# Performance work log

Hardware: AMD Instinct MI355X
Metric: run time of the kernel (lower is better)

Reference implementation:

```python
import jax, jax.numpy as jnp
import numpy as np

LN_EPS = 1e-5


def setup_inputs() -> dict:
    key = jax.random.key(0)
    ks = jax.random.split(key, 6)
    B, I, H = 16384, 512, 512
    x = jax.random.normal(ks[0], (B, I), dtype=jnp.float32)
    h_prev = jax.random.normal(ks[1], (B, H), dtype=jnp.float32)
    c_prev = jax.random.normal(ks[2], (B, H), dtype=jnp.float32)
    # packed gate weights in i|f|g|o order (equivalent to 8 separate matmuls)
    W_i = jax.random.normal(ks[3], (I, 4 * H), dtype=jnp.float32) * (1.0 / np.sqrt(I))
    W_h = jax.random.normal(ks[4], (H, 4 * H), dtype=jnp.float32) * (1.0 / np.sqrt(H))
    # biases: b_i=0, b_f=1, b_g=0, b_o=0 as in the torch module
    b = jnp.concatenate([jnp.zeros(H), jnp.ones(H), jnp.zeros(H), jnp.zeros(H)]).astype(jnp.float32)
    ln_weight = jnp.ones((H,), dtype=jnp.float32)
    ln_bias = jnp.zeros((H,), dtype=jnp.float32)
    return {"x": x, "h_prev": h_prev, "c_prev": c_prev, "W_i": W_i, "W_h": W_h,
            "b": b, "ln_weight": ln_weight, "ln_bias": ln_bias}


def layer_norm(h, w, bias):
    mu = jnp.mean(h, axis=-1, keepdims=True)
    var = jnp.var(h, axis=-1, keepdims=True)
    return (h - mu) * jax.lax.rsqrt(var + LN_EPS) * w + bias


def reference(x, h_prev, c_prev, W_i, W_h, b, ln_weight, ln_bias):
    H = h_prev.shape[-1]
    # two fused GEMMs covering all 4 gates: [B, 4H]
    gates = x @ W_i + h_prev @ W_h + b
    i, f, g, o = jnp.split(gates, 4, axis=-1)
    i = jax.nn.sigmoid(i)
    f = jax.nn.sigmoid(f)
    g = jnp.tanh(g)
    o = jax.nn.sigmoid(o)
    c = f * c_prev + i * g
    h = o * jnp.tanh(c)
    h = layer_norm(h, ln_weight, ln_bias)
    return (h, c)
```

## Files before the change

kernel.cpp:

```cpp
#include <hip/hip_runtime.h>
#include <cstdint>
#include <cstddef>

typedef unsigned short ushort_t;
typedef __attribute__((ext_vector_type(8))) short bf16x8;
typedef __attribute__((ext_vector_type(4))) float f32x4;

#define MROWS 16384
#define KDIM  1024
#define NDIM  2048
#define HDIM  512

static __device__ __forceinline__ unsigned short f2bf(float f) {
    unsigned int u = __float_as_uint(f);
    u += 0x7fffu + ((u >> 16) & 1u);
    return (unsigned short)(u >> 16);
}

static __device__ __forceinline__ float sigmoid_f(float x) {
    return 1.0f / (1.0f + __expf(-x));
}
static __device__ __forceinline__ float tanh_f(float x) {
    float t = __expf(2.0f * x);
    return 1.0f - 2.0f / (t + 1.0f);
}

__global__ __launch_bounds__(256) void pack_ab(const float* __restrict__ x,
                                               const float* __restrict__ hp,
                                               const float* __restrict__ Wi,
                                               const float* __restrict__ Wh,
                                               ushort_t* __restrict__ A,
                                               ushort_t* __restrict__ Bt) {
    __shared__ ushort_t sm[64][72];
    const int tid = threadIdx.x;
    if (blockIdx.x < 8192) {
        int t = blockIdx.x * 256 + tid;
        int row = t >> 7;
        int kc = (t & 127) << 3;
        const float* src = (kc < 512) ? (x + (size_t)row * 512 + kc)
                                      : (hp + (size_t)row * 512 + (kc - 512));
        float4 v0 = ((const float4*)src)[0];
        float4 v1 = ((const float4*)src)[1];
        ushort_t o[8] __attribute__((aligned(16)));
        o[0] = f2bf(v0.x); o[1] = f2bf(v0.y); o[2] = f2bf(v0.z); o[3] = f2bf(v0.w);
        o[4] = f2bf(v1.x); o[5] = f2bf(v1.y); o[6] = f2bf(v1.z); o[7] = f2bf(v1.w);
        *((uint4*)(A + (size_t)row * KDIM + kc)) = *((const uint4*)o);
    } else {
        int b2 = blockIdx.x - 8192;
        int kt = b2 >> 5;
        int ct = b2 & 31;
        const float* W = (kt < 8) ? (Wi + (size_t)(kt * 64) * NDIM)
                                  : (Wh + (size_t)((kt - 8) * 64) * NDIM);
        int c0 = (tid & 15) * 4;
        int r0 = tid >> 4;
#pragma unroll
        for (int r = 0; r < 4; ++r) {
            int krow = r * 16 + r0;
            float4 v = *((const float4*)(W + (size_t)krow * NDIM + ct * 64 + c0));
            sm[krow][c0 + 0] = f2bf(v.x);
            sm[krow][c0 + 1] = f2bf(v.y);
            sm[krow][c0 + 2] = f2bf(v.z);
            sm[krow][c0 + 3] = f2bf(v.w);
        }
        __syncthreads();
        int g = (ct * 64) >> 9;
        int h0 = ct * 64 - g * 512;
#pragma unroll
        for (int q = tid; q < 512; q += 256) {
            int cc = q >> 3;
            int kc = (q & 7) * 8;
            ushort_t o[8] __attribute__((aligned(16)));
#pragma unroll
            for (int j = 0; j < 8; ++j) o[j] = sm[kc + j][cc];
            int np = 4 * (h0 + cc) + g;
            *((uint4*)(Bt + (size_t)np * KDIM + kt * 64 + kc)) = *((const uint4*)o);
        }
    }
}

__global__ __launch_bounds__(256) void gemm_cell(const ushort_t* __restrict__ A,
                                                 const ushort_t* __restrict__ Bt,
                                                 const float* __restrict__ b,
                                                 const float* __restrict__ c_prev,
                                                 float* __restrict__ h_out,
                                                 float* __restrict__ c_out) {
    __shared__ float smem_f[8192];
    ushort_t* Als = (ushort_t*)smem_f;
    ushort_t* Bls = Als + 128 * 64;

    const int tid  = threadIdx.x;
    const int w    = tid >> 6;
    const int lane = tid & 63;
    const int n0 = blockIdx.x * 128;
    const int m0 = blockIdx.y * 128;
    const int wm = (w >> 1) * 64;
    const int wn = (w & 1) * 64;
    const int lr   = lane & 15;
    const int quad = lane >> 4;
    const int sw   = lr & 7;

    f32x4 zero = {0.f, 0.f, 0.f, 0.f};
    f32x4 acc[4][4];
#pragma unroll
    for (int i = 0; i < 4; ++i)
#pragma unroll
        for (int j = 0; j < 4; ++j) acc[i][j] = zero;

    for (int kt = 0; kt < KDIM / 64; ++kt) {
#pragma unroll
        for (int r = 0; r < 4; ++r) {
            int c = r * 256 + tid;
            int trow = c >> 3;
            int chg = (c & 7) ^ (trow & 7);
            const ushort_t* ga = A + (size_t)(m0 + trow) * KDIM + kt * 64 + chg * 8;
            __builtin_amdgcn_global_load_lds(
                (const __attribute__((address_space(1))) void*)ga,
                (__attribute__((address_space(3))) void*)((char*)Als + c * 16),
                16, 0, 0);
            const ushort_t* gb = Bt + (size_t)(n0 + trow) * KDIM + kt * 64 + chg * 8;
            __builtin_amdgcn_global_load_lds(
                (const __attribute__((address_space(1))) void*)gb,
                (__attribute__((address_space(3))) void*)((char*)Bls + c * 16),
                16, 0, 0);
        }
        __syncthreads();

#pragma unroll
        for (int kk = 0; kk < 2; ++kk) {
            bf16x8 af[4], bf[4];
#pragma unroll
            for (int t2 = 0; t2 < 4; ++t2) {
                int ra = wm + t2 * 16 + lr;
                int rb = wn + t2 * 16 + lr;
                int ch = kk * 4 + quad;
                af[t2] = *((const bf16x8*)(Als + (ra * 8 + (ch ^ sw)) * 8));
                bf[t2] = *((const bf16x8*)(Bls + (rb * 8 + (ch ^ sw)) * 8));
            }
#pragma unroll
            for (int tm = 0; tm < 4; ++tm)
#pragma unroll
                for (int tn = 0; tn < 4; ++tn)
                    acc[tm][tn] = __builtin_amdgcn_mfma_f32_16x16x32_bf16(
                        af[tm], bf[tn], acc[tm][tn], 0, 0, 0);
        }
        __syncthreads();
    }

#pragma unroll
    for (int half = 0; half < 2; ++half) {
        __syncthreads();
        if ((w >> 1) == half) {
#pragma unroll
            for (int tm = 0; tm < 4; ++tm) {
                int rl = tm * 16 + quad * 4;
#pragma unroll
                for (int tn = 0; tn < 4; ++tn) {
                    int cl = wn + tn * 16 + lr;
#pragma unroll
                    for (int rg = 0; rg < 4; ++rg)
                        smem_f[(rl + rg) * 128 + cl] = acc[tm][tn][rg];
                }
            }
        }
        __syncthreads();
#pragma unroll
        for (int ii = 0; ii < 8; ++ii) {
            int item = ii * 256 + tid;
            int rloc = item >> 5;
            int hloc = item & 31;
            float4 gv = *((const float4*)(smem_f + rloc * 128 + hloc * 4));
            int grow = m0 + half * 64 + rloc;
            int hg = (n0 >> 2) + hloc;
            float iv = sigmoid_f(gv.x + b[hg]);
            float fv = sigmoid_f(gv.y + b[512 + hg]);
            float g2 = tanh_f(gv.z + b[1024 + hg]);
            float ov = sigmoid_f(gv.w + b[1536 + hg]);
            float cp = c_prev[(size_t)grow * HDIM + hg];
            float cn = fv * cp + iv * g2;
            float hr = ov * tanh_f(cn);
            c_out[(size_t)grow * HDIM + hg] = cn;
            h_out[(size_t)grow * HDIM + hg] = hr;
        }
    }
}

__global__ __launch_bounds__(256) void ln_kernel(float* __restrict__ h,
                                                 const float* __restrict__ lw,
                                                 const float* __restrict__ lb) {
    int w = threadIdx.x >> 6;
    int lane = threadIdx.x & 63;
    int row = blockIdx.x * 4 + w;
    float* p = h + (size_t)row * HDIM + lane * 8;
    float4 a = ((const float4*)p)[0];
    float4 c = ((const float4*)p)[1];
    float s  = a.x + a.y + a.z + a.w + c.x + c.y + c.z + c.w;
    float ss = a.x * a.x + a.y * a.y + a.z * a.z + a.w * a.w +
               c.x * c.x + c.y * c.y + c.z * c.z + c.w * c.w;
#pragma unroll
    for (int off = 32; off > 0; off >>= 1) {
        s  += __shfl_xor(s, off);
        ss += __shfl_xor(ss, off);
    }
    float mu = s * (1.0f / 512.0f);
    float var = ss * (1.0f / 512.0f) - mu * mu;
    float rstd = rsqrtf(var + 1e-5f);
    const float* wp = lw + lane * 8;
    const float* bp = lb + lane * 8;
    float4 w0 = ((const float4*)wp)[0];
    float4 w1 = ((const float4*)wp)[1];
    float4 b0 = ((const float4*)bp)[0];
    float4 b1 = ((const float4*)bp)[1];
    a.x = (a.x - mu) * rstd * w0.x + b0.x;
    a.y = (a.y - mu) * rstd * w0.y + b0.y;
    a.z = (a.z - mu) * rstd * w0.z + b0.z;
    a.w = (a.w - mu) * rstd * w0.w + b0.w;
    c.x = (c.x - mu) * rstd * w1.x + b1.x;
    c.y = (c.y - mu) * rstd * w1.y + b1.y;
    c.z = (c.z - mu) * rstd * w1.z + b1.z;
    c.w = (c.w - mu) * rstd * w1.w + b1.w;
    ((float4*)p)[0] = a;
    ((float4*)p)[1] = c;
}

extern "C" void kernel_launch(void* const* d_in, const int* in_sizes, int n_in,
                              void* d_out, int out_size, void* d_ws, size_t ws_size,
                              hipStream_t stream) {
    const float* x      = (const float*)d_in[0];
    const float* h_prev = (const float*)d_in[1];
    const float* c_prev = (const float*)d_in[2];
    const float* W_i    = (const float*)d_in[3];
    const float* W_h    = (const float*)d_in[4];
    const float* b      = (const float*)d_in[5];
    const float* ln_w   = (const float*)d_in[6];
    const float* ln_b   = (const float*)d_in[7];

    float* h_out = (float*)d_out;
    float* c_out = h_out + (size_t)MROWS * HDIM;

    ushort_t* A  = (ushort_t*)d_ws;
    ushort_t* Bt = A + (size_t)MROWS * KDIM;

    pack_ab<<<8192 + 512, 256, 0, stream>>>(x, h_prev, W_i, W_h, A, Bt);
    dim3 grid(NDIM / 128, MROWS / 128);
    gemm_cell<<<grid, 256, 0, stream>>>(A, Bt, b, c_prev, h_out, c_out);
    ln_kernel<<<MROWS / 4, 256, 0, stream>>>(h_out, ln_w, ln_b);
}
```

Baseline: 286.0 us.

## Shrink GEMM tile to 128x64 with XCD-aware block remap and per-wave epilogue

Changes the gate GEMM tile from 128x128 to 128x64, which halves the accumulators per wave, cuts LDS use and sets launch bounds for four blocks per CU to raise occupancy. A 1D grid is remapped so that consecutive blocks on the same XCD share A rows, aiming at better L2 reuse. The epilogue now runs per wave through a swizzled private scratch area with no block-wide syncs, and uses vectorized float4 loads and stores for bias, c_prev and the outputs. In exchange, each A tile is reloaded twice as often across N tiles, which lowers arithmetic intensity per block.

```diff
diff --git a/kernel.cpp b/kernel.cpp
--- a/kernel.cpp
+++ b/kernel.cpp
@@ -78,33 +78,35 @@
     }
 }
 
-__global__ __launch_bounds__(256) void gemm_cell(const ushort_t* __restrict__ A,
-                                                 const ushort_t* __restrict__ Bt,
-                                                 const float* __restrict__ b,
-                                                 const float* __restrict__ c_prev,
-                                                 float* __restrict__ h_out,
-                                                 float* __restrict__ c_out) {
-    __shared__ float smem_f[8192];
+__global__ __launch_bounds__(256, 4) void gemm_cell(const ushort_t* __restrict__ A,
+                                                    const ushort_t* __restrict__ Bt,
+                                                    const float* __restrict__ b,
+                                                    const float* __restrict__ c_prev,
+                                                    float* __restrict__ h_out,
+                                                    float* __restrict__ c_out) {
+    __shared__ float smem_f[6144];
     ushort_t* Als = (ushort_t*)smem_f;
     ushort_t* Bls = Als + 128 * 64;
 
     const int tid  = threadIdx.x;
     const int w    = tid >> 6;
     const int lane = tid & 63;
-    const int n0 = blockIdx.x * 128;
-    const int m0 = blockIdx.y * 128;
+    int bid = blockIdx.x;
+    int lid = (bid >> 3) + (bid & 7) * 512;
+    const int m0 = (lid >> 5) * 128;
+    const int n0 = (lid & 31) * 64;
     const int wm = (w >> 1) * 64;
-    const int wn = (w & 1) * 64;
+    const int wn = (w & 1) * 32;
     const int lr   = lane & 15;
     const int quad = lane >> 4;
     const int sw   = lr & 7;
 
     f32x4 zero = {0.f, 0.f, 0.f, 0.f};
-    f32x4 acc[4][4];
+    f32x4 acc[4][2];
 #pragma unroll
     for (int i = 0; i < 4; ++i)
 #pragma unroll
-        for (int j = 0; j < 4; ++j) acc[i][j] = zero;
+        for (int j = 0; j < 2; ++j) acc[i][j] = zero;
 
     for (int kt = 0; kt < KDIM / 64; ++kt) {
 #pragma unroll
@@ -117,6 +119,12 @@
                 (const __attribute__((address_space(1))) void*)ga,
                 (__attribute__((address_space(3))) void*)((char*)Als + c * 16),
                 16, 0, 0);
+        }
+#pragma unroll
+        for (int r = 0; r < 2; ++r) {
+            int c = r * 256 + tid;
+            int trow = c >> 3;
+            int chg = (c & 7) ^ (trow & 7);
             const ushort_t* gb = Bt + (size_t)(n0 + trow) * KDIM + kt * 64 + chg * 8;
             __builtin_amdgcn_global_load_lds(
                 (const __attribute__((address_space(1))) void*)gb,
@@ -127,60 +135,81 @@
 
 #pragma unroll
         for (int kk = 0; kk < 2; ++kk) {
-            bf16x8 af[4], bf[4];
+            bf16x8 af[4], bf[2];
+            int ch = kk * 4 + quad;
 #pragma unroll
             for (int t2 = 0; t2 < 4; ++t2) {
                 int ra = wm + t2 * 16 + lr;
+                af[t2] = *((const bf16x8*)(Als + (ra * 8 + (ch ^ sw)) * 8));
+            }
+#pragma unroll
+            for (int t2 = 0; t2 < 2; ++t2) {
                 int rb = wn + t2 * 16 + lr;
-                int ch = kk * 4 + quad;
-                af[t2] = *((const bf16x8*)(Als + (ra * 8 + (ch ^ sw)) * 8));
                 bf[t2] = *((const bf16x8*)(Bls + (rb * 8 + (ch ^ sw)) * 8));
             }
 #pragma unroll
             for (int tm = 0; tm < 4; ++tm)
 #pragma unroll
-                for (int tn = 0; tn < 4; ++tn)
+                for (int tn = 0; tn < 2; ++tn)
                     acc[tm][tn] = __builtin_amdgcn_mfma_f32_16x16x32_bf16(
                         af[tm], bf[tn], acc[tm][tn], 0, 0, 0);
         }
         __syncthreads();
     }
 
-#pragma unroll
-    for (int half = 0; half < 2; ++half) {
-        __syncthreads();
-        if ((w >> 1) == half) {
-#pragma unroll
-            for (int tm = 0; tm < 4; ++tm) {
-                int rl = tm * 16 + quad * 4;
-#pragma unroll
-                for (int tn = 0; tn < 4; ++tn) {
-                    int cl = wn + tn * 16 + lr;
-#pragma unroll
-                    for (int rg = 0; rg < 4; ++rg)
-                        smem_f[(rl + rg) * 128 + cl] = acc[tm][tn][rg];
+    float* scr = smem_f + w * 1024;
+    const int hg0 = ((n0 + wn) >> 2) + ((lane & 1) << 2);
+    const float4 bi4 = *((const float4*)(b + hg0));
+    const float4 bf4 = *((const float4*)(b + 512 + hg0));
+    const float4 bg4 = *((const float4*)(b + 1024 + hg0));
+    const float4 bo4 = *((const float4*)(b + 1536 + hg0));
+    const int rr = lane >> 1;
+
+#pragma unroll
+    for (int chunk = 0; chunk < 2; ++chunk) {
+#pragma unroll
+        for (int tm2 = 0; tm2 < 2; ++tm2) {
+            int tm = chunk * 2 + tm2;
+#pragma unroll
+            for (int tn = 0; tn < 2; ++tn) {
+                int c = tn * 16 + lr;
+#pragma unroll
+                for (int rg = 0; rg < 4; ++rg) {
+                    int r = tm2 * 16 + quad * 4 + rg;
+                    int blk = (c >> 2) ^ (r & 7);
+                    scr[r * 32 + blk * 4 + (c & 3)] = acc[tm][tn][rg];
                 }
             }
         }
-        __syncthreads();
-#pragma unroll
-        for (int ii = 0; ii < 8; ++ii) {
-            int item = ii * 256 + tid;
-            int rloc = item >> 5;
-            int hloc = item & 31;
-            float4 gv = *((const float4*)(smem_f + rloc * 128 + hloc * 4));
-            int grow = m0 + half * 64 + rloc;
-            int hg = (n0 >> 2) + hloc;
-            float iv = sigmoid_f(gv.x + b[hg]);
-            float fv = sigmoid_f(gv.y + b[512 + hg]);
-            float g2 = tanh_f(gv.z + b[1024 + hg]);
-            float ov = sigmoid_f(gv.w + b[1536 + hg]);
-            float cp = c_prev[(size_t)grow * HDIM + hg];
-            float cn = fv * cp + iv * g2;
-            float hr = ov * tanh_f(cn);
-            c_out[(size_t)grow * HDIM + hg] = cn;
-            h_out[(size_t)grow * HDIM + hg] = hr;
-        }
+        float4 gv[4];
+#pragma unroll
+        for (int j = 0; j < 4; ++j) {
+            int hg_l = ((lane & 1) << 2) + j;
+            int blk = hg_l ^ (rr & 7);
+            gv[j] = *((const float4*)(scr + rr * 32 + blk * 4));
+        }
+        int grow = m0 + wm + chunk * 32 + rr;
+        float4 cp = *((const float4*)(c_prev + (size_t)grow * HDIM + hg0));
+        float cn[4], hv[4];
+        {
+            float iv, fv, g2, ov;
+            iv = sigmoid_f(gv[0].x + bi4.x); fv = sigmoid_f(gv[0].y + bf4.x);
+            g2 = tanh_f(gv[0].z + bg4.x);    ov = sigmoid_f(gv[0].w + bo4.x);
+            cn[0] = fv * cp.x + iv * g2;     hv[0] = ov * tanh_f(cn[0]);
+            iv = sigmoid_f(gv[1].x + bi4.y); fv = sigmoid_f(gv[1].y + bf4.y);
+            g2 = tanh_f(gv[1].z + bg4.y);    ov = sigmoid_f(gv[1].w + bo4.y);
+            cn[1] = fv * cp.y + iv * g2;     hv[1] = ov * tanh_f(cn[1]);
+            iv = sigmoid_f(gv[2].x + bi4.z); fv = sigmoid_f(gv[2].y + bf4.z);
+            g2 = tanh_f(gv[2].z + bg4.z);    ov = sigmoid_f(gv[2].w + bo4.z);
+            cn[2] = fv * cp.z + iv * g2;     hv[2] = ov * tanh_f(cn[2]);
+            iv = sigmoid_f(gv[3].x + bi4.w); fv = sigmoid_f(gv[3].y + bf4.w);
+            g2 = tanh_f(gv[3].z + bg4.w);    ov = sigmoid_f(gv[3].w + bo4.w);
+            cn[3] = fv * cp.w + iv * g2;     hv[3] = ov * tanh_f(cn[3]);
+        }
+        float4 cno = {cn[0], cn[1], cn[2], cn[3]};
+        float4 hvo = {hv[0], hv[1], hv[2], hv[3]};
+        *((float4*)(c_out + (size_t)grow * HDIM + hg0)) = cno;
+        *((float4*)(h_out + (size_t)grow * HDIM + hg0)) = hvo;
     }
 }
 
@@ -241,7 +270,6 @@
     ushort_t* Bt = A + (size_t)MROWS * KDIM;
 
     pack_ab<<<8192 + 512, 256, 0, stream>>>(x, h_prev, W_i, W_h, A, Bt);
-    dim3 grid(NDIM / 128, MROWS / 128);
-    gemm_cell<<<grid, 256, 0, stream>>>(A, Bt, b, c_prev, h_out, c_out);
+    gemm_cell<<<4096, 256, 0, stream>>>(A, Bt, b, c_prev, h_out, c_out);
     ln_kernel<<<MROWS / 4, 256, 0, stream>>>(h_out, ln_w, ln_b);
 }
```

Measured after the change: 257.0 us. -10.1%, faster.
